# Performance work log

Measured on AMD Instinct MI355X. Metric: run time of the kernel, lower is better.

Reference implementation:

```python
import jax, jax.numpy as jnp
import numpy as np

B, N = 2, 131072          # batch, expanded node slots (divisible by flag_size)
FEAT = 69                 # org(3) + pos(3) + uids(63)
KERNELS = 128
FLAG_SIZE = 4             # 1 << dims, dims = 2
BINS = 16                 # 1 << flag_size


def _conv1d(x, w, b, stride=1, padding='SAME'):
    # keras Conv1D: x [B,N,Cin], w [K,Cin,Cout], relu activation
    y = jax.lax.conv_general_dilated(x, w, (stride,), padding,
                                     dimension_numbers=('NWC', 'WIO', 'NWC'))
    return jax.nn.relu(y + b)


def setup_inputs() -> dict:
    key = jax.random.key(0)
    ks = jax.random.split(key, 12)

    def g(k, shape):
        fan_in = int(np.prod(shape[:-1]))
        return (jax.random.normal(k, shape, jnp.float32) / np.sqrt(fan_in)).astype(jnp.float32)

    c_x = FEAT + KERNELS                 # 197 after each pre conv concat
    c_flags = 2 * FEAT + KERNELS         # 266 flags-head input
    c_sym = c_flags + FLAG_SIZE          # 270 symbols-branch input

    return {
        'inputs': jax.random.normal(ks[0], (B, N, FEAT), jnp.float32),
        'w_pre0': g(ks[1], (3, FEAT, KERNELS)),   'b_pre0': jnp.zeros((KERNELS,), jnp.float32),
        'w_pre1': g(ks[2], (3, c_x, KERNELS)),    'b_pre1': jnp.zeros((KERNELS,), jnp.float32),
        'w_flags': g(ks[3], (c_flags, FLAG_SIZE)), 'b_flags': jnp.zeros((FLAG_SIZE,), jnp.float32),
        'w_merge': g(ks[4], (FLAG_SIZE, c_sym, KERNELS)), 'b_merge': jnp.zeros((KERNELS,), jnp.float32),
        'w_post0': g(ks[5], (3, KERNELS, KERNELS)), 'b_post0': jnp.zeros((KERNELS,), jnp.float32),
        'w_post1': g(ks[6], (3, KERNELS, KERNELS)), 'b_post1': jnp.zeros((KERNELS,), jnp.float32),
        'w_post2': g(ks[7], (3, KERNELS, KERNELS)), 'b_post2': jnp.zeros((KERNELS,), jnp.float32),
        'w_post3': g(ks[8], (3, KERNELS, KERNELS)), 'b_post3': jnp.zeros((KERNELS,), jnp.float32),
        'w_sym': g(ks[9], (KERNELS, BINS)),        'b_sym': jnp.zeros((BINS,), jnp.float32),
    }


def _forward(inputs, w_pre0, b_pre0, w_pre1, b_pre1, w_flags, b_flags,
             w_merge, b_merge, w_post0, b_post0, w_post1, b_post1,
             w_post2, b_post2, w_post3, b_post3, w_sym, b_sym):
    # pos offsets = (3, 6); pos = inputs[..., 3:5] (2 columns)
    pos = inputs[..., 3:5]
    sort = jnp.argsort(pos, axis=-2)                       # [B, N, 2]
    # gather with batch_dims=1 along node axis
    X = jnp.take_along_axis(inputs, sort[..., 1:2], axis=1)   # sorted by pos col 1
    x0 = jax.lax.stop_gradient(X)                            # [B, N, 69]
    X = jnp.concatenate([x0, _conv1d(X, w_pre0, b_pre0)], axis=-1)  # [B, N, 197]
    X = jnp.concatenate([x0, _conv1d(X, w_pre1, b_pre1)], axis=-1)  # [B, N, 197]
    X = jnp.concatenate([X, jnp.take_along_axis(inputs, sort[..., 0:1], axis=1)], axis=-1)  # [B, N, 266]

    F = jax.nn.sigmoid(X @ w_flags + b_flags)               # [B, N, 4]

    S = jax.lax.stop_gradient(jnp.concatenate([F, X], axis=-1))     # [B, N, 270]
    S = _conv1d(S, w_merge, b_merge, stride=FLAG_SIZE, padding='VALID')  # [B, N/4, 128]
    for w, b in ((w_post0, b_post0), (w_post1, b_post1), (w_post2, b_post2), (w_post3, b_post3)):
        S = _conv1d(S, w, b)
    S = jax.nn.softmax(S @ w_sym + b_sym, axis=-1)          # [B, N/4, 16]

    Fd = (F[..., 0] - F[..., 1]).reshape(F.shape[0], -1, FLAG_SIZE)  # [B, N/4, 4]
    return jnp.concatenate([Fd, S], axis=-1)                # [B, N/4, 20]


def reference(inputs, w_pre0, b_pre0, w_pre1, b_pre1, w_flags, b_flags,
              w_merge, b_merge, w_post0, b_post0, w_post1, b_post1,
              w_post2, b_post2, w_post3, b_post3, w_sym, b_sym):
    return _forward(inputs, w_pre0, b_pre0, w_pre1, b_pre1, w_flags, b_flags,
                    w_merge, b_merge, w_post0, b_post0, w_post1, b_post1,
                    w_post2, b_post2, w_post3, b_post3, w_sym, b_sym)
```

## Files before the change

### kernel.cpp

```cpp
#include <hip/hip_runtime.h>
#include <hip/hip_bf16.h>
#include <math.h>

#define NPOS 131072
#define NF   69
#define NMRG 32768
#define TILE 2048
#define TPS  64
#define NSORT 4

typedef __attribute__((ext_vector_type(8))) short short8;
typedef __bf16 bf16x8 __attribute__((ext_vector_type(8)));
typedef __attribute__((ext_vector_type(4))) float f32x4;

static __device__ inline bf16x8 as_bf16x8(short8 v){ union{short8 s; bf16x8 b;} u; u.s=v; return u.b; }
static __device__ inline short f2bf(float x){ __hip_bfloat16 h = __float2bfloat16(x); return *(short*)&h; }
static __device__ inline float bf2f(short s){ return __uint_as_float(((unsigned)(unsigned short)s)<<16); }

static __device__ inline void gld16(const short* g, short* l){
  __builtin_amdgcn_global_load_lds(
      (const __attribute__((address_space(1))) unsigned int*)g,
      (__attribute__((address_space(3))) unsigned int*)l, 16, 0, 0);
}

__global__ void k_make_keys(const float* __restrict__ inp, unsigned* __restrict__ kA,
                            unsigned* __restrict__ vA){
  unsigned t = blockIdx.x*256u + threadIdx.x;
  unsigned s = t >> 17, i = t & (NPOS-1u);
  unsigned b = s >> 1, ch = 3u + (s & 1u);
  float x = inp[((size_t)b*NPOS + i)*NF + ch];
  unsigned u = __float_as_uint(x);
  u = (u & 0x80000000u) ? ~u : (u | 0x80000000u);
  kA[t] = u; vA[t] = i;
}

__global__ __launch_bounds__(256) void k_hist(const unsigned* __restrict__ src,
                                              unsigned* __restrict__ hist, int shift){
  __shared__ unsigned h[256];
  int tid = threadIdx.x;
  h[tid] = 0u; __syncthreads();
  int s = blockIdx.x / TPS, tile = blockIdx.x % TPS;
  const unsigned* ks = src + (size_t)s*NPOS + (size_t)tile*TILE;
  for (int r = 0; r < TILE/256; ++r){
    unsigned d = (ks[r*256 + tid] >> shift) & 255u;
    atomicAdd(&h[d], 1u);
  }
  __syncthreads();
  hist[s*16384 + tid*TPS + tile] = h[tid];
}

__global__ __launch_bounds__(256) void k_scan(unsigned* __restrict__ hist){
  __shared__ unsigned tot[256];
  int tid = threadIdx.x; int s = blockIdx.x;
  unsigned* g = hist + s*16384;
  unsigned sum = 0;
  for (int q = 0; q < 64; ++q) sum += g[tid*64 + q];
  tot[tid] = sum;
  __syncthreads();
  if (tid == 0){
    unsigned run = 0;
    for (int t = 0; t < 256; ++t){ unsigned tmp = tot[t]; tot[t] = run; run += tmp; }
  }
  __syncthreads();
  unsigned run = tot[tid];
  for (int q = 0; q < 64; ++q){ unsigned tmp = g[tid*64+q]; g[tid*64+q] = run; run += tmp; }
}

#define EPT 16
__global__ __launch_bounds__(128) void k_scatter(const unsigned* __restrict__ srcK,
    const unsigned* __restrict__ srcV, unsigned* __restrict__ dstK, unsigned* __restrict__ dstV,
    const unsigned* __restrict__ off, int shift){
  __shared__ unsigned short cnt[256*128];
  int tid = threadIdx.x;
  unsigned* cz = (unsigned*)cnt;
  for (int idx = tid; idx < 256*128/2; idx += 128) cz[idx] = 0u;
  __syncthreads();
  int s = blockIdx.x / TPS, tile = blockIdx.x % TPS;
  const unsigned* ks = srcK + (size_t)s*NPOS + (size_t)tile*TILE;
  const unsigned* vs = srcV + (size_t)s*NPOS + (size_t)tile*TILE;
  unsigned k8[EPT], v8[EPT];
  #pragma unroll
  for (int r = 0; r < EPT; ++r){
    k8[r] = ks[tid*EPT + r];
    v8[r] = vs[tid*EPT + r];
    unsigned d = (k8[r] >> shift) & 255u;
    cnt[d*128 + tid]++;
  }
  __syncthreads();
  for (int dd = 0; dd < 2; ++dd){
    int d = tid + dd*128;
    unsigned run = 0;
    for (int t = 0; t < 128; ++t){ unsigned tmp = cnt[d*128 + t]; cnt[d*128 + t] = (unsigned short)run; run += tmp; }
  }
  __syncthreads();
  const unsigned* ob = off + s*16384;
  #pragma unroll
  for (int r = 0; r < EPT; ++r){
    unsigned d = (k8[r] >> shift) & 255u;
    unsigned rk = cnt[d*128 + tid];
    cnt[d*128 + tid] = (unsigned short)(rk + 1u);
    unsigned pos = ob[d*TPS + tile] + rk;
    dstK[(size_t)s*NPOS + pos] = k8[r];
    dstV[(size_t)s*NPOS + pos] = v8[r];
  }
}

__global__ __launch_bounds__(256) void k_gath(const float* __restrict__ inp,
    const unsigned* __restrict__ P1, const unsigned* __restrict__ P0,
    short* __restrict__ XA, short* __restrict__ Xcat, int b){
  int t = blockIdx.x*256 + threadIdx.x;
  int i = t >> 7, c = t & 127;
  if (c < 69){
    short s1 = f2bf(inp[((size_t)b*NPOS + P1[i])*NF + c]);
    XA[(size_t)i*224 + 128 + c] = s1;
    Xcat[(size_t)i*272 + 132 + c] = s1;
    Xcat[(size_t)i*272 + 201 + c] = f2bf(inp[((size_t)b*NPOS + P0[i])*NF + c]);
  } else if (c == 69){
    Xcat[(size_t)i*272 + 270] = 0;
    Xcat[(size_t)i*272 + 271] = 0;
  }
}

__global__ void k_prepB(const float* __restrict__ w, short* __restrict__ out,
                        int KC, int mode, int total){
  int t = blockIdx.x*256 + threadIdx.x;
  if (t >= total) return;
  int kv = t & 7, nn = (t>>3) & 127, cc = (t>>10) % KC, tap = (t>>10) / KC;
  int kc16 = kv ^ (nn & 7);
  short o[8];
  #pragma unroll
  for (int e = 0; e < 8; ++e){
    int ch = cc*64 + kc16*8 + e;
    float val = 0.f;
    if (mode == 0){ if (ch < 69)  val = w[((size_t)tap*69  + ch)*128 + nn]; }
    else if (mode == 1){
      if (ch < 128)      val = w[((size_t)tap*197 + 69 + ch)*128 + nn];
      else if (ch < 197) val = w[((size_t)tap*197 + ch - 128)*128 + nn];
    }
    else if (mode == 2){ if (ch < 128) val = w[((size_t)tap*128 + ch)*128 + nn]; }
    else {
      int tm = ch / 272, cm = ch - tm*272;
      int orig = -1;
      if (cm < 128)      orig = 73 + cm;
      else if (cm < 201) orig = cm - 128;
      else if (cm < 270) orig = cm;
      if (orig >= 0) val = w[((size_t)tm*270 + orig)*128 + nn];
    }
    o[e] = f2bf(val);
  }
  *(short8*)(out + (size_t)t*8) = *(short8*)o;
}

__global__ void k_prepWf(const float* __restrict__ wf, float* __restrict__ out){
  int t = blockIdx.x*256 + threadIdx.x;
  if (t >= 1088) return;
  int c = t >> 2, q = t & 3;
  float v = 0.f;
  if (c < 128)                 v = wf[(69 + c)*4 + q];
  else if (c >= 132 && c < 201) v = wf[(c - 132)*4 + q];
  else if (c >= 201 && c < 270) v = wf[(197 + c - 201)*4 + q];
  out[t] = v;
}

#define OSTR 132

template<int CPAD>
__global__ __launch_bounds__(256) void k_conv3r(
    const short* __restrict__ src, int sstride, int coff, int cin,
    const short* __restrict__ wB, const float* __restrict__ bias,
    short* __restrict__ dst, int dstride, int n)
{
  constexpr int KC = CPAD/64;
  constexpr int ASTR = CPAD + 8;
  constexpr int AG = CPAD/8;
  constexpr size_t ABYTES = (size_t)66*ASTR*2;
  constexpr size_t OBYTES = (size_t)64*OSTR*4;
  constexpr size_t LBYTES = (ABYTES > OBYTES) ? ABYTES : OBYTES;
  __shared__ __attribute__((aligned(16))) char LDS[LBYTES];
  short* A_s = (short*)LDS;
  float* OT  = (float*)LDS;
  int tid = threadIdx.x;
  int i0 = blockIdx.x*64;
  int wv = tid >> 6, lane = tid & 63;
  int lm = lane & 15, lk = lane >> 4;

  for (int idx = tid; idx < 66*AG; idx += 256){
    int r = idx / AG, g = idx - r*AG;
    int pos = i0 - 1 + r;
    short8 v = {0,0,0,0,0,0,0,0};
    if (pos >= 0 && pos < n && g*8 < cin){
      const short* sp = src + (size_t)pos*sstride + coff + g*8;
      if (g*8 + 8 <= cin) v = *(const short8*)sp;
      else { for (int j = 0; g*8 + j < cin; ++j) v[j] = sp[j]; }
    }
    *(short8*)(A_s + r*ASTR + g*8) = v;
  }
  __syncthreads();

  f32x4 acc[4][2] = {};
  #pragma unroll
  for (int tp = 0; tp < 3; ++tp){
    bf16x8 bfr[KC][2][2];
    #pragma unroll
    for (int c = 0; c < KC; ++c)
      #pragma unroll
      for (int ksub = 0; ksub < 2; ++ksub)
        #pragma unroll
        for (int ni = 0; ni < 2; ++ni){
          int nn = wv*32 + ni*16 + lm;
          bfr[c][ksub][ni] = as_bf16x8(*(const short8*)(
              wB + (size_t)(tp*KC + c)*8192 + nn*64 + (((ksub*4+lk) ^ (nn&7))*8)));
        }
    #pragma unroll
    for (int c = 0; c < KC; ++c){
      #pragma unroll
      for (int ksub = 0; ksub < 2; ++ksub){
        bf16x8 a[4];
        #pragma unroll
        for (int mi = 0; mi < 4; ++mi)
          a[mi] = as_bf16x8(*(const short8*)(A_s + (mi*16+lm+tp)*ASTR + c*64 + ksub*32 + lk*8));
        #pragma unroll
        for (int mi = 0; mi < 4; ++mi)
          #pragma unroll
          for (int ni = 0; ni < 2; ++ni)
            acc[mi][ni] = __builtin_amdgcn_mfma_f32_16x16x32_bf16(a[mi], bfr[c][ksub][ni], acc[mi][ni], 0, 0, 0);
      }
    }
  }
  __syncthreads();
  float b0 = bias[wv*32 + lm], b1 = bias[wv*32 + 16 + lm];
  #pragma unroll
  for (int mi = 0; mi < 4; ++mi)
    #pragma unroll
    for (int ni = 0; ni < 2; ++ni){
      float bb = ni ? b1 : b0;
      #pragma unroll
      for (int r = 0; r < 4; ++r)
        OT[(mi*16 + lk*4 + r)*OSTR + wv*32 + ni*16 + lm] = fmaxf(acc[mi][ni][r] + bb, 0.f);
    }
  __syncthreads();
  {
    int r = tid >> 2, q = tid & 3;
    const float* row = OT + r*OSTR + q*32;
    short o[32];
    #pragma unroll
    for (int jc = 0; jc < 8; ++jc){
      f32x4 v = *(const f32x4*)(row + jc*4);
      #pragma unroll
      for (int e = 0; e < 4; ++e) o[jc*4+e] = f2bf(v[e]);
    }
    short* dp = dst + (size_t)(i0 + r)*dstride + q*32;
    #pragma unroll
    for (int v8 = 0; v8 < 4; ++v8) *(short8*)(dp + v8*8) = *(short8*)(o + v8*8);
  }
}

__global__ __launch_bounds__(256) void k_mergem2(const short* __restrict__ Xf,
    const short* __restrict__ wB, const float* __restrict__ bias, short* __restrict__ dst)
{
  constexpr size_t ABYTES = 2*4096*2;
  constexpr size_t BBYTES = 2*8192*2;
  __shared__ __attribute__((aligned(16))) char LDS[ABYTES + BBYTES];
  short* A_s = (short*)LDS;
  short* B_s = (short*)(LDS + ABYTES);
  float* OT  = (float*)LDS;
  int tid = threadIdx.x;
  int j0 = blockIdx.x*64;
  auto stageA = [&](int s){
    #pragma unroll
    for (int it = 0; it < 2; ++it){
      int slot = it*256 + tid;
      int r = slot >> 3, kv = slot & 7;
      const short* gp = Xf + (size_t)(j0 + r)*1088 + s*64 + ((kv ^ (r&7))*8);
      gld16(gp, A_s + (s&1)*4096 + slot*8);
    }
  };
  auto stageB = [&](int s){
    const short* gp = wB + (size_t)s*8192 + tid*8;
    short* lp = B_s + (s&1)*8192 + tid*8;
    #pragma unroll
    for (int it = 0; it < 4; ++it) gld16(gp + it*2048, lp + it*2048);
  };
  stageA(0); stageB(0);
  __syncthreads();
  int wv = tid >> 6, lane = tid & 63;
  int lm = lane & 15, lk = lane >> 4;
  f32x4 acc[4][2] = {};
  for (int s = 0; s < 17; ++s){
    if (s+1 < 17){ stageA(s+1); stageB(s+1); }
    const short* Ab = A_s + (s&1)*4096;
    const short* Bb = B_s + (s&1)*8192;
    #pragma unroll
    for (int ksub = 0; ksub < 2; ++ksub){
      bf16x8 a[4], b[2];
      #pragma unroll
      for (int mi = 0; mi < 4; ++mi){
        int r = mi*16 + lm;
        a[mi] = as_bf16x8(*(const short8*)(Ab + r*64 + (((ksub*4+lk) ^ (r&7))*8)));
      }
      #pragma unroll
      for (int ni = 0; ni < 2; ++ni){
        int nn = wv*32 + ni*16 + lm;
        b[ni] = as_bf16x8(*(const short8*)(Bb + nn*64 + (((ksub*4+lk) ^ (nn&7))*8)));
      }
      #pragma unroll
      for (int mi = 0; mi < 4; ++mi)
        #pragma unroll
        for (int ni = 0; ni < 2; ++ni)
          acc[mi][ni] = __builtin_amdgcn_mfma_f32_16x16x32_bf16(a[mi], b[ni], acc[mi][ni], 0, 0, 0);
    }
    __syncthreads();
  }
  float b0 = bias[wv*32 + lm], b1 = bias[wv*32 + 16 + lm];
  #pragma unroll
  for (int mi = 0; mi < 4; ++mi)
    #pragma unroll
    for (int ni = 0; ni < 2; ++ni){
      float bb = ni ? b1 : b0;
      #pragma unroll
      for (int r = 0; r < 4; ++r)
        OT[(mi*16 + lk*4 + r)*OSTR + wv*32 + ni*16 + lm] = fmaxf(acc[mi][ni][r] + bb, 0.f);
    }
  __syncthreads();
  {
    int r = tid >> 2, q = tid & 3;
    const float* row = OT + r*OSTR + q*32;
    short o[32];
    #pragma unroll
    for (int jc = 0; jc < 8; ++jc){
      f32x4 v = *(const f32x4*)(row + jc*4);
      #pragma unroll
      for (int e = 0; e < 4; ++e) o[jc*4+e] = f2bf(v[e]);
    }
    short* dp = dst + (size_t)(j0 + r)*128 + q*32;
    #pragma unroll
    for (int v8 = 0; v8 < 4; ++v8) *(short8*)(dp + v8*8) = *(short8*)(o + v8*8);
  }
}

__global__ __launch_bounds__(256) void k_flags2(short* __restrict__ Xcat,
    const float* __restrict__ Wf2, const float* __restrict__ bf, float* __restrict__ F){
  size_t i = (size_t)blockIdx.x*256 + threadIdx.x;
  const short* x = Xcat + i*272;
  float a0 = bf[0], a1 = bf[1], a2 = bf[2], a3 = bf[3];
  for (int g = 0; g < 34; ++g){
    short8 x8 = *(const short8*)(x + g*8);
    #pragma unroll
    for (int e = 0; e < 8; ++e){
      float xv = bf2f(x8[e]);
      const float* w = Wf2 + (g*8+e)*4;
      a0 = fmaf(xv,w[0],a0); a1 = fmaf(xv,w[1],a1); a2 = fmaf(xv,w[2],a2); a3 = fmaf(xv,w[3],a3);
    }
  }
  float f0 = 1.f/(1.f+expf(-a0)), f1 = 1.f/(1.f+expf(-a1));
  float f2 = 1.f/(1.f+expf(-a2)), f3 = 1.f/(1.f+expf(-a3));
  float* f = F + i*4;
  f[0]=f0; f[1]=f1; f[2]=f2; f[3]=f3;
  short* xc = Xcat + i*272 + 128;
  xc[0]=f2bf(f0); xc[1]=f2bf(f1); xc[2]=f2bf(f2); xc[3]=f2bf(f3);
}

__global__ __launch_bounds__(256) void k_out(const short* __restrict__ S,
    const float* __restrict__ F, const float* __restrict__ Ws, const float* __restrict__ bs,
    float* __restrict__ out, int b){
  size_t j = (size_t)blockIdx.x*256 + threadIdx.x;
  float l[16];
  #pragma unroll
  for (int t = 0; t < 16; ++t) l[t] = bs[t];
  const short* s = S + j*128;
  for (int g = 0; g < 16; ++g){
    short8 x8 = *(const short8*)(s + g*8);
    #pragma unroll
    for (int e = 0; e < 8; ++e){
      float x = bf2f(x8[e]);
      const float* w = Ws + (g*8+e)*16;
      #pragma unroll
      for (int t = 0; t < 16; ++t) l[t] = fmaf(x, w[t], l[t]);
    }
  }
  float m = l[0];
  #pragma unroll
  for (int t = 1; t < 16; ++t) m = fmaxf(m, l[t]);
  float sum = 0.f;
  #pragma unroll
  for (int t = 0; t < 16; ++t){ l[t] = expf(l[t]-m); sum += l[t]; }
  float inv = 1.f/sum;
  float* o = out + ((size_t)b*NMRG + j)*20;
  #pragma unroll
  for (int k = 0; k < 4; ++k){
    size_t r = (size_t)(4*j + k)*4;
    o[k] = F[r] - F[r+1];
  }
  #pragma unroll
  for (int t = 0; t < 16; ++t) o[4+t] = l[t]*inv;
}

extern "C" void kernel_launch(void* const* d_in, const int* in_sizes, int n_in,
                              void* d_out, int out_size, void* d_ws, size_t ws_size,
                              hipStream_t stream){
  const float* inp     = (const float*)d_in[0];
  const float* w_pre0  = (const float*)d_in[1];
  const float* b_pre0  = (const float*)d_in[2];
  const float* w_pre1  = (const float*)d_in[3];
  const float* b_pre1  = (const float*)d_in[4];
  const float* w_flags = (const float*)d_in[5];
  const float* b_flags = (const float*)d_in[6];
  const float* w_merge = (const float*)d_in[7];
  const float* b_merge = (const float*)d_in[8];
  const float* w_post[4] = {(const float*)d_in[9], (const float*)d_in[11],
                            (const float*)d_in[13], (const float*)d_in[15]};
  const float* b_post[4] = {(const float*)d_in[10], (const float*)d_in[12],
                            (const float*)d_in[14], (const float*)d_in[16]};
  const float* w_sym   = (const float*)d_in[17];
  const float* b_sym   = (const float*)d_in[18];
  float* outp = (float*)d_out;

  char* p = (char*)d_ws;
  unsigned* kA = (unsigned*)p; p += (size_t)NSORT*NPOS*4;
  unsigned* vA = (unsigned*)p; p += (size_t)NSORT*NPOS*4;
  unsigned* kB = (unsigned*)p; p += (size_t)NSORT*NPOS*4;
  unsigned* vB = (unsigned*)p; p += (size_t)NSORT*NPOS*4;
  unsigned* hist = (unsigned*)p; p += (size_t)NSORT*16384*4;
  short* XA   = (short*)p; p += (size_t)NPOS*224*2;
  short* Xcat = (short*)p; p += (size_t)NPOS*272*2;
  float* Fbuf = (float*)p; p += (size_t)NPOS*4*4;
  short* M0   = (short*)p; p += (size_t)NMRG*128*2;
  short* M1   = (short*)p; p += (size_t)NMRG*128*2;
  short* wb0  = (short*)p; p += (size_t)3*2*8192*2;
  short* wb1  = (short*)p; p += (size_t)3*4*8192*2;
  short* wbq0 = (short*)p; p += (size_t)3*2*8192*2;
  short* wbq1 = (short*)p; p += (size_t)3*2*8192*2;
  short* wbq2 = (short*)p; p += (size_t)3*2*8192*2;
  short* wbq3 = (short*)p; p += (size_t)3*2*8192*2;
  short* wbm  = (short*)p; p += (size_t)17*8192*2;
  float* wf2  = (float*)p; p += (size_t)272*4*4;
  if ((size_t)(p - (char*)d_ws) > ws_size) return;
  short* wbq[4] = {wbq0, wbq1, wbq2, wbq3};

  k_prepB<<<(3*2*1024+255)/256, 256, 0, stream>>>(w_pre0, wb0, 2, 0, 3*2*1024);
  k_prepB<<<(3*4*1024+255)/256, 256, 0, stream>>>(w_pre1, wb1, 4, 1, 3*4*1024);
  for (int i = 0; i < 4; ++i)
    k_prepB<<<(3*2*1024+255)/256, 256, 0, stream>>>(w_post[i], wbq[i], 2, 2, 3*2*1024);
  k_prepB<<<(17*1024+255)/256, 256, 0, stream>>>(w_merge, wbm, 17, 3, 17*1024);
  k_prepWf<<<5, 256, 0, stream>>>(w_flags, wf2);

  k_make_keys<<<NSORT*NPOS/256, 256, 0, stream>>>(inp, kA, vA);
  unsigned *sk = kA, *sv = vA, *dk = kB, *dv = vB;
  for (int pass = 0; pass < 4; ++pass){
    int shift = pass*8;
    k_hist<<<NSORT*TPS, 256, 0, stream>>>(sk, hist, shift);
    k_scan<<<NSORT, 256, 0, stream>>>(hist);
    k_scatter<<<NSORT*TPS, 128, 0, stream>>>(sk, sv, dk, dv, hist, shift);
    unsigned* t;
    t = sk; sk = dk; dk = t;
    t = sv; sv = dv; dv = t;
  }
  for (int b = 0; b < 2; ++b){
    const unsigned* P0 = sv + (size_t)(b*2+0)*NPOS;
    const unsigned* P1 = sv + (size_t)(b*2+1)*NPOS;
    k_gath<<<NPOS*128/256, 256, 0, stream>>>(inp, P1, P0, XA, Xcat, b);
    k_conv3r<128><<<NPOS/64, 256, 0, stream>>>(XA, 224, 128, 69,  wb0, b_pre0, XA,   224, NPOS);
    k_conv3r<256><<<NPOS/64, 256, 0, stream>>>(XA, 224, 0,   197, wb1, b_pre1, Xcat, 272, NPOS);
    k_flags2<<<NPOS/256, 256, 0, stream>>>(Xcat, wf2, b_flags, Fbuf);
    k_mergem2<<<NMRG/64, 256, 0, stream>>>(Xcat, wbm, b_merge, M0);
    k_conv3r<128><<<NMRG/64, 256, 0, stream>>>(M0, 128, 0, 128, wbq[0], b_post[0], M1, 128, NMRG);
    k_conv3r<128><<<NMRG/64, 256, 0, stream>>>(M1, 128, 0, 128, wbq[1], b_post[1], M0, 128, NMRG);
    k_conv3r<128><<<NMRG/64, 256, 0, stream>>>(M0, 128, 0, 128, wbq[2], b_post[2], M1, 128, NMRG);
    k_conv3r<128><<<NMRG/64, 256, 0, stream>>>(M1, 128, 0, 128, wbq[3], b_post[3], M0, 128, NMRG);
    k_out<<<NMRG/256, 256, 0, stream>>>(M0, Fbuf, w_sym, b_sym, outp, b);
  }
}
```

Measured before the change: 612.5 us.

## Pre-swizzle weights into per-lane fragment order and load directly to registers

```diff
diff --git a/kernel.cpp b/kernel.cpp
--- a/kernel.cpp
+++ b/kernel.cpp
@@ -122,15 +122,20 @@
 }
 
 __global__ void k_prepB(const float* __restrict__ w, short* __restrict__ out,
-                        int KC, int mode, int total){
+                        int KC, int NQ, int mode, int total){
   int t = blockIdx.x*256 + threadIdx.x;
   if (t >= total) return;
-  int kv = t & 7, nn = (t>>3) & 127, cc = (t>>10) % KC, tap = (t>>10) / KC;
-  int kc16 = kv ^ (nn & 7);
+  int lane = t & 63, ni = (t>>6) & 1, ksub = (t>>7) & 1;
+  int rest = t >> 8;
+  int q = rest % NQ;
+  int wv = rest / NQ;
+  int tap = q / KC, cc = q - tap*KC;
+  int nn = wv*32 + ni*16 + (lane & 15);
+  int chb = cc*64 + ksub*32 + ((lane >> 4) & 3)*8;
   short o[8];
   #pragma unroll
   for (int e = 0; e < 8; ++e){
-    int ch = cc*64 + kc16*8 + e;
+    int ch = chb + e;
     float val = 0.f;
     if (mode == 0){ if (ch < 69)  val = w[((size_t)tap*69  + ch)*128 + nn]; }
     else if (mode == 1){
@@ -171,6 +176,7 @@
     short* __restrict__ dst, int dstride, int n)
 {
   constexpr int KC = CPAD/64;
+  constexpr int NSTEP = 3*KC;
   constexpr int ASTR = CPAD + 8;
   constexpr int AG = CPAD/8;
   constexpr size_t ABYTES = (size_t)66*ASTR*2;
@@ -197,6 +203,7 @@
   }
   __syncthreads();
 
+  const short* wBw = wB + (size_t)wv*NSTEP*2048 + (size_t)lane*8;
   f32x4 acc[4][2] = {};
   #pragma unroll
   for (int tp = 0; tp < 3; ++tp){
@@ -206,11 +213,9 @@
       #pragma unroll
       for (int ksub = 0; ksub < 2; ++ksub)
         #pragma unroll
-        for (int ni = 0; ni < 2; ++ni){
-          int nn = wv*32 + ni*16 + lm;
+        for (int ni = 0; ni < 2; ++ni)
           bfr[c][ksub][ni] = as_bf16x8(*(const short8*)(
-              wB + (size_t)(tp*KC + c)*8192 + nn*64 + (((ksub*4+lk) ^ (nn&7))*8)));
-        }
+              wBw + (((size_t)(tp*KC + c)*2 + ksub)*2 + ni)*512));
     #pragma unroll
     for (int c = 0; c < KC; ++c){
       #pragma unroll
@@ -255,17 +260,17 @@
   }
 }
 
-__global__ __launch_bounds__(256) void k_mergem2(const short* __restrict__ Xf,
+__global__ __launch_bounds__(256) void k_mergem3(const short* __restrict__ Xf,
     const short* __restrict__ wB, const float* __restrict__ bias, short* __restrict__ dst)
 {
-  constexpr size_t ABYTES = 2*4096*2;
-  constexpr size_t BBYTES = 2*8192*2;
-  __shared__ __attribute__((aligned(16))) char LDS[ABYTES + BBYTES];
+  constexpr size_t OBYTES = (size_t)64*OSTR*4;
+  __shared__ __attribute__((aligned(16))) char LDS[OBYTES];
   short* A_s = (short*)LDS;
-  short* B_s = (short*)(LDS + ABYTES);
   float* OT  = (float*)LDS;
   int tid = threadIdx.x;
   int j0 = blockIdx.x*64;
+  int wv = tid >> 6, lane = tid & 63;
+  int lm = lane & 15, lk = lane >> 4;
   auto stageA = [&](int s){
     #pragma unroll
     for (int it = 0; it < 2; ++it){
@@ -275,41 +280,44 @@
       gld16(gp, A_s + (s&1)*4096 + slot*8);
     }
   };
-  auto stageB = [&](int s){
-    const short* gp = wB + (size_t)s*8192 + tid*8;
-    short* lp = B_s + (s&1)*8192 + tid*8;
-    #pragma unroll
-    for (int it = 0; it < 4; ++it) gld16(gp + it*2048, lp + it*2048);
+  const short* wBl = wB + (size_t)wv*17*2048 + (size_t)lane*8;
+  auto LB = [&](int s, int ks, int ni){
+    return as_bf16x8(*(const short8*)(wBl + ((size_t)(s*2 + ks)*2 + ni)*512));
   };
-  stageA(0); stageB(0);
-  __syncthreads();
-  int wv = tid >> 6, lane = tid & 63;
-  int lm = lane & 15, lk = lane >> 4;
+  bf16x8 c00 = LB(0,0,0), c01 = LB(0,0,1), c10 = LB(0,1,0), c11 = LB(0,1,1);
+  stageA(0);
+  __syncthreads();
   f32x4 acc[4][2] = {};
   for (int s = 0; s < 17; ++s){
-    if (s+1 < 17){ stageA(s+1); stageB(s+1); }
+    bf16x8 n00, n01, n10, n11;
+    if (s < 16){
+      n00 = LB(s+1,0,0); n01 = LB(s+1,0,1); n10 = LB(s+1,1,0); n11 = LB(s+1,1,1);
+      stageA(s+1);
+    }
     const short* Ab = A_s + (s&1)*4096;
-    const short* Bb = B_s + (s&1)*8192;
-    #pragma unroll
-    for (int ksub = 0; ksub < 2; ++ksub){
-      bf16x8 a[4], b[2];
-      #pragma unroll
-      for (int mi = 0; mi < 4; ++mi){
-        int r = mi*16 + lm;
-        a[mi] = as_bf16x8(*(const short8*)(Ab + r*64 + (((ksub*4+lk) ^ (r&7))*8)));
-      }
-      #pragma unroll
-      for (int ni = 0; ni < 2; ++ni){
-        int nn = wv*32 + ni*16 + lm;
-        b[ni] = as_bf16x8(*(const short8*)(Bb + nn*64 + (((ksub*4+lk) ^ (nn&7))*8)));
-      }
-      #pragma unroll
-      for (int mi = 0; mi < 4; ++mi)
-        #pragma unroll
-        for (int ni = 0; ni < 2; ++ni)
-          acc[mi][ni] = __builtin_amdgcn_mfma_f32_16x16x32_bf16(a[mi], b[ni], acc[mi][ni], 0, 0, 0);
+    bf16x8 a[4];
+    #pragma unroll
+    for (int mi = 0; mi < 4; ++mi){
+      int r = mi*16 + lm;
+      a[mi] = as_bf16x8(*(const short8*)(Ab + r*64 + ((lk ^ (r&7))*8)));
+    }
+    #pragma unroll
+    for (int mi = 0; mi < 4; ++mi){
+      acc[mi][0] = __builtin_amdgcn_mfma_f32_16x16x32_bf16(a[mi], c00, acc[mi][0], 0, 0, 0);
+      acc[mi][1] = __builtin_amdgcn_mfma_f32_16x16x32_bf16(a[mi], c01, acc[mi][1], 0, 0, 0);
+    }
+    #pragma unroll
+    for (int mi = 0; mi < 4; ++mi){
+      int r = mi*16 + lm;
+      a[mi] = as_bf16x8(*(const short8*)(Ab + r*64 + (((4+lk) ^ (r&7))*8)));
+    }
+    #pragma unroll
+    for (int mi = 0; mi < 4; ++mi){
+      acc[mi][0] = __builtin_amdgcn_mfma_f32_16x16x32_bf16(a[mi], c10, acc[mi][0], 0, 0, 0);
+      acc[mi][1] = __builtin_amdgcn_mfma_f32_16x16x32_bf16(a[mi], c11, acc[mi][1], 0, 0, 0);
     }
     __syncthreads();
+    c00 = n00; c01 = n01; c10 = n10; c11 = n11;
   }
   float b0 = bias[wv*32 + lm], b1 = bias[wv*32 + 16 + lm];
   #pragma unroll
@@ -437,11 +445,11 @@
   if ((size_t)(p - (char*)d_ws) > ws_size) return;
   short* wbq[4] = {wbq0, wbq1, wbq2, wbq3};
 
-  k_prepB<<<(3*2*1024+255)/256, 256, 0, stream>>>(w_pre0, wb0, 2, 0, 3*2*1024);
-  k_prepB<<<(3*4*1024+255)/256, 256, 0, stream>>>(w_pre1, wb1, 4, 1, 3*4*1024);
+  k_prepB<<<(6144 +255)/256, 256, 0, stream>>>(w_pre0, wb0, 2, 6, 0, 6144);
+  k_prepB<<<(12288+255)/256, 256, 0, stream>>>(w_pre1, wb1, 4, 12, 1, 12288);
   for (int i = 0; i < 4; ++i)
-    k_prepB<<<(3*2*1024+255)/256, 256, 0, stream>>>(w_post[i], wbq[i], 2, 2, 3*2*1024);
-  k_prepB<<<(17*1024+255)/256, 256, 0, stream>>>(w_merge, wbm, 17, 3, 17*1024);
+    k_prepB<<<(6144+255)/256, 256, 0, stream>>>(w_post[i], wbq[i], 2, 6, 2, 6144);
+  k_prepB<<<(17408+255)/256, 256, 0, stream>>>(w_merge, wbm, 17, 17, 3, 17408);
   k_prepWf<<<5, 256, 0, stream>>>(w_flags, wf2);
 
   k_make_keys<<<NSORT*NPOS/256, 256, 0, stream>>>(inp, kA, vA);
@@ -462,7 +470,7 @@
     k_conv3r<128><<<NPOS/64, 256, 0, stream>>>(XA, 224, 128, 69,  wb0, b_pre0, XA,   224, NPOS);
     k_conv3r<256><<<NPOS/64, 256, 0, stream>>>(XA, 224, 0,   197, wb1, b_pre1, Xcat, 272, NPOS);
     k_flags2<<<NPOS/256, 256, 0, stream>>>(Xcat, wf2, b_flags, Fbuf);
-    k_mergem2<<<NMRG/64, 256, 0, stream>>>(Xcat, wbm, b_merge, M0);
+    k_mergem3<<<NMRG/64, 256, 0, stream>>>(Xcat, wbm, b_merge, M0);
     k_conv3r<128><<<NMRG/64, 256, 0, stream>>>(M0, 128, 0, 128, wbq[0], b_post[0], M1, 128, NMRG);
     k_conv3r<128><<<NMRG/64, 256, 0, stream>>>(M1, 128, 0, 128, wbq[1], b_post[1], M0, 128, NMRG);
     k_conv3r<128><<<NMRG/64, 256, 0, stream>>>(M0, 128, 0, 128, wbq[2], b_post[2], M1, 128, NMRG);
```

Result: faster. 596.5 us (-2.6%).
